# Performance work log

Measured on AMD Instinct MI355X. Metric: run time of the kernel, lower is better.

The kernel has to match this reference:

```python
import jax, jax.numpy as jnp
import numpy as np

HIDDEN = 4096
N_HEADS = 32
N_KV_HEADS = 8
HEAD_SIZE = HIDDEN // N_HEADS  # 128
ROPE_THETA = 10000.0
SEQ_LEN = 1024
BATCH = 4


def setup_inputs() -> dict:
    key = jax.random.key(0)
    k1, k2, k3 = jax.random.split(key, 3)
    scale = 1.0 / np.sqrt(HIDDEN)
    hidden_states = jax.random.normal(k1, (BATCH * SEQ_LEN, HIDDEN), dtype=jnp.float32)
    w_qkv = jax.random.normal(k2, ((N_HEADS + 2 * N_KV_HEADS) * HEAD_SIZE, HIDDEN), dtype=jnp.float32) * scale
    w_o = jax.random.normal(k3, (HIDDEN, N_HEADS * HEAD_SIZE), dtype=jnp.float32) * scale
    return {"hidden_states": hidden_states, "w_qkv": w_qkv, "w_o": w_o, "seq_len": SEQ_LEN}


def _rope(x, pos, theta):
    # x: [B, S, H, D]; pos: [S] absolute positions; rotate-half (LLAMA/NeoX) style
    d = x.shape[-1]
    inv_freq = 1.0 / (theta ** (jnp.arange(0, d, 2, dtype=jnp.float32) / d))  # [D/2]
    ang = pos.astype(jnp.float32)[:, None] * inv_freq[None, :]  # [S, D/2]
    cos = jnp.cos(ang)[None, :, None, :]
    sin = jnp.sin(ang)[None, :, None, :]
    x1, x2 = jnp.split(x, 2, axis=-1)
    return jnp.concatenate([x1 * cos - x2 * sin, x2 * cos + x1 * sin], axis=-1)


def reference(hidden_states, w_qkv, w_o, seq_len):
    total, hidden = hidden_states.shape
    B = total // seq_len
    hd = HEAD_SIZE
    # fused QKV projection (bias-free), split like the torch module
    qkv = hidden_states @ w_qkv.T  # [T, (H+2K)*hd]
    q, k, v = jnp.split(qkv, [N_HEADS * hd, (N_HEADS + N_KV_HEADS) * hd], axis=1)
    q = q.reshape(B, seq_len, N_HEADS, hd)
    k = k.reshape(B, seq_len, N_KV_HEADS, hd)
    v = v.reshape(B, seq_len, N_KV_HEADS, hd)
    # inline RoPE (ROPE_LLAMA) on q and k at absolute positions
    pos = jnp.arange(seq_len)
    q = _rope(q, pos, ROPE_THETA)
    k = _rope(k, pos, ROPE_THETA)
    # GQA: map each q head to its kv head (kv_head_mapping = repeat_interleave)
    groups = N_HEADS // N_KV_HEADS
    k = jnp.repeat(k, groups, axis=2)  # [B, S, H, hd]
    v = jnp.repeat(v, groups, axis=2)
    scale = hd ** -0.5
    scores = jnp.einsum('bqhd,bkhd->bhqk', q, k) * scale  # [B, H, S, S]
    causal = jnp.tril(jnp.ones((seq_len, seq_len), dtype=bool))
    scores = jnp.where(causal[None, None], scores, jnp.finfo(scores.dtype).min)
    probs = jax.nn.softmax(scores, axis=-1)
    attn = jnp.einsum('bhqk,bkhd->bqhd', probs, v).reshape(total, N_HEADS * hd)
    return attn @ w_o.T  # [T, hidden]
```

## Files before the change

kernel.cpp:

```cpp
#include <hip/hip_runtime.h>


typedef short bf16x8 __attribute__((ext_vector_type(8)));
typedef short bf16x4 __attribute__((ext_vector_type(4)));
typedef float floatx4 __attribute__((ext_vector_type(4)));
typedef unsigned short u16x8 __attribute__((ext_vector_type(8)));

__device__ __forceinline__ unsigned short f2bf(float f) {
  unsigned u = __float_as_uint(f);
  u += 0x7FFFu + ((u >> 16) & 1u);
  return (unsigned short)(u >> 16);
}
__device__ __forceinline__ float bf2f(unsigned short h) {
  return __uint_as_float(((unsigned)h) << 16);
}

__device__ __forceinline__ void async16(const void* g, void* l) {
  __builtin_amdgcn_global_load_lds(
      (const __attribute__((address_space(1))) unsigned int*)g,
      (__attribute__((address_space(3))) unsigned int*)l, 16, 0, 0);
}

__global__ void cvt_f32_bf16(const float4* __restrict__ in,
                             u16x8* __restrict__ out, int n8) {
  int i = blockIdx.x * 256 + threadIdx.x;
  if (i < n8) {
    float4 a = in[2 * i], b = in[2 * i + 1];
    u16x8 o;
    o[0] = f2bf(a.x); o[1] = f2bf(a.y); o[2] = f2bf(a.z); o[3] = f2bf(a.w);
    o[4] = f2bf(b.x); o[5] = f2bf(b.y); o[6] = f2bf(b.z); o[7] = f2bf(b.w);
    out[i] = o;
  }
}

template <int OUT_BF16>
__global__ __launch_bounds__(512, 2) void gemm256(
    const unsigned short* __restrict__ A, const unsigned short* __restrict__ B,
    void* __restrict__ Cout, int M, int N, int K, int n0) {
  __shared__ __align__(16) unsigned short As[4][8192];
  __shared__ __align__(16) unsigned short Bs[4][8192];
  const int tid = threadIdx.x;
  const int wave = tid >> 6, lane = tid & 63;
  const int wm = wave >> 2, wn = wave & 3;
  const int l16 = lane & 15, c4 = lane >> 4;
  const int bm = blockIdx.y << 8, bn = (blockIdx.x << 8) + n0;

  int afOff[8], bfOff[4];
#pragma unroll
  for (int mi = 0; mi < 8; ++mi) {
    int r = wm * 128 + mi * 16 + l16;
    int pr = r >> 1, l8 = ((r & 1) << 2) | c4;
    afOff[mi] = pr * 128 + ((l8 ^ (pr & 7)) << 4);
  }
#pragma unroll
  for (int ni = 0; ni < 4; ++ni) {
    int r = wn * 64 + ni * 16 + l16;
    int pr = r >> 1, l8 = ((r & 1) << 2) | c4;
    bfOff[ni] = pr * 128 + ((l8 ^ (pr & 7)) << 4);
  }

  const int sp = lane >> 3;
  const int l8s = (lane & 7) ^ sp;
  const int so = l8s >> 2, sc = (l8s & 3) << 3;
  const unsigned short* aS0 = A + (size_t)(bm + wave * 16 + sp * 2 + so) * K + sc;
  const unsigned short* aS1 = A + (size_t)(bm + (wave + 8) * 16 + sp * 2 + so) * K + sc;
  const unsigned short* bS0 = B + (size_t)(bn + wave * 16 + sp * 2 + so) * K + sc;
  const unsigned short* bS1 = B + (size_t)(bn + (wave + 8) * 16 + sp * 2 + so) * K + sc;
  const int dst0 = wave * 1024, dst1 = (wave + 8) * 1024;

  floatx4 acc[8][4];
#pragma unroll
  for (int mi = 0; mi < 8; ++mi)
#pragma unroll
    for (int ni = 0; ni < 4; ++ni) acc[mi][ni] = (floatx4){0.f, 0.f, 0.f, 0.f};

  const int NT = K >> 5;
  async16(aS0, (char*)As[0] + dst0);
  async16(aS1, (char*)As[0] + dst1);
  async16(bS0, (char*)Bs[0] + dst0);
  async16(bS1, (char*)Bs[0] + dst1);
  async16(aS0 + 32, (char*)As[1] + dst0);
  async16(aS1 + 32, (char*)As[1] + dst1);
  async16(bS0 + 32, (char*)Bs[1] + dst0);
  async16(bS1 + 32, (char*)Bs[1] + dst1);
  asm volatile("s_waitcnt vmcnt(4)" ::: "memory");
  __builtin_amdgcn_s_barrier();

  bf16x8 afq0[4], afq1[4], bfcA[4], bfcB[4];
#pragma unroll
  for (int i = 0; i < 4; ++i)
    afq0[i] = *(const bf16x8*)((const char*)As[0] + afOff[i]);
#pragma unroll
  for (int i = 0; i < 4; ++i)
    bfcA[i] = *(const bf16x8*)((const char*)Bs[0] + bfOff[i]);

  size_t koff = 64;

#define KTILE(T, BC, BN_)                                                     \
  {                                                                           \
    const char* aB = (const char*)As[(T) & 3];                                \
    const char* aN = (const char*)As[((T) + 1) & 3];                          \
    const char* bN = (const char*)Bs[((T) + 1) & 3];                          \
    char* aD = (char*)As[((T) + 2) & 3];                                      \
    char* bD = (char*)Bs[((T) + 2) & 3];                                      \
    _Pragma("unroll") for (int i = 0; i < 4; ++i)                             \
        afq1[i] = *(const bf16x8*)(aB + afOff[4 + i]);                        \
    async16(aS0 + koff, aD + dst0);                                           \
    async16(aS1 + koff, aD + dst1);                                           \
    __builtin_amdgcn_s_barrier();                                             \
    __builtin_amdgcn_s_setprio(1);                                            \
    _Pragma("unroll") for (int mi = 0; mi < 4; ++mi)                          \
        _Pragma("unroll") for (int ni = 0; ni < 4; ++ni)                      \
            acc[mi][ni] = __builtin_amdgcn_mfma_f32_16x16x32_bf16(            \
                afq0[mi], BC[ni], acc[mi][ni], 0, 0, 0);                      \
    __builtin_amdgcn_s_setprio(0);                                            \
    asm volatile("s_waitcnt vmcnt(2)" ::: "memory");   \
    __builtin_amdgcn_s_barrier();                     \
    _Pragma("unroll") for (int i = 0; i < 4; ++i)                             \
        afq0[i] = *(const bf16x8*)(aN + afOff[i]);                            \
    _Pragma("unroll") for (int i = 0; i < 4; ++i)                             \
        BN_[i] = *(const bf16x8*)(bN + bfOff[i]);                             \
    async16(bS0 + koff, bD + dst0);                                           \
    async16(bS1 + koff, bD + dst1);                                           \
    __builtin_amdgcn_s_barrier();                                             \
    __builtin_amdgcn_s_setprio(1);                                            \
    _Pragma("unroll") for (int mi = 0; mi < 4; ++mi)                          \
        _Pragma("unroll") for (int ni = 0; ni < 4; ++ni)                      \
            acc[4 + mi][ni] = __builtin_amdgcn_mfma_f32_16x16x32_bf16(        \
                afq1[mi], BC[ni], acc[4 + mi][ni], 0, 0, 0);                  \
    __builtin_amdgcn_s_setprio(0);                                            \
    __builtin_amdgcn_s_barrier();                                             \
    koff += 32;                                                               \
  }

  for (int t = 0; t < NT; t += 2) {
    KTILE(t, bfcA, bfcB);
    KTILE(t + 1, bfcB, bfcA);
  }
#undef KTILE

  const int col0 = bn + wn * 64 + l16;
#pragma unroll
  for (int mi = 0; mi < 8; ++mi) {
    const int row0 = bm + wm * 128 + mi * 16 + c4 * 4;
#pragma unroll
    for (int ni = 0; ni < 4; ++ni)
#pragma unroll
      for (int r = 0; r < 4; ++r) {
        if (OUT_BF16)
          ((unsigned short*)Cout)[(size_t)(row0 + r) * N + col0 + ni * 16] =
              f2bf(acc[mi][ni][r]);
        else
          ((float*)Cout)[(size_t)(row0 + r) * N + col0 + ni * 16] =
              acc[mi][ni][r];
      }
  }
}

__global__ void rope_k_kernel(unsigned short* __restrict__ qkv) {
  const int t = blockIdx.x;
  const int s = t & 1023;
  const int head = 32 + blockIdx.y * 4 + (threadIdx.x >> 6);
  const int d = threadIdx.x & 63;
  unsigned short* p = qkv + (size_t)t * 6144 + head * 128;
  float x1 = bf2f(p[d]), x2 = bf2f(p[d + 64]);
  float inv_freq = exp2f((float)d * -0.20762050593046015f);
  float ang = (float)s * inv_freq;
  float c, sn;
  __sincosf(ang, &sn, &c);
  p[d] = f2bf(x1 * c - x2 * sn);
  p[d + 64] = f2bf(x2 * c + x1 * sn);
}

__global__ __launch_bounds__(256, 3) void flash_attn(
    const unsigned short* __restrict__ qkv, unsigned short* __restrict__ aout) {
  const int pr = blockIdx.x;
  const int h = blockIdx.y, b = blockIdx.z;
  const int kh = h >> 2;
  const int tid = threadIdx.x;
  const int wave = tid >> 6, lane = tid & 63;
  const int quad = lane >> 4, l16 = lane & 15;

  __shared__ __align__(16) unsigned short Ks[64][136];
  __shared__ __align__(16) unsigned short Vt[128][68];
  __shared__ __align__(16) unsigned short Ps[64][68];

  const int krow = tid >> 4, kcol = (tid & 15) << 3;
  const int vrb = (tid & 15) << 2, vcol = (tid >> 4) << 3;
  const unsigned short* kp = qkv + (size_t)(b << 10) * 6144 + 4096 + kh * 128;
  const unsigned short* vp = qkv + (size_t)(b << 10) * 6144 + 5120 + kh * 128;

  for (int half = 0; half < 2; ++half) {
    const int qt = half ? pr : 15 - pr;
    const int q0 = qt << 6;

    bf16x8 qf[4];
    {
      const int qrow = q0 + wave * 16 + l16;
      const unsigned short* qp =
          qkv + (size_t)((b << 10) + qrow) * 6144 + h * 128 + quad * 8;
#pragma unroll
      for (int ks = 0; ks < 4; ++ks) qf[ks] = *(const bf16x8*)(qp + ks * 32);
      const float pos = (float)qrow;
      const float scale = 0.08838834764831845f;
#pragma unroll
      for (int ks = 0; ks < 2; ++ks)
#pragma unroll
        for (int e = 0; e < 8; ++e) {
          int d = ks * 32 + quad * 8 + e;
          float ang = pos * exp2f((float)d * -0.20762050593046015f);
          float c, sn;
          __sincosf(ang, &sn, &c);
          float x1 = bf2f((unsigned short)qf[ks][e]);
          float x2 = bf2f((unsigned short)qf[ks + 2][e]);
          qf[ks][e] = (short)f2bf((x1 * c - x2 * sn) * scale);
          qf[ks + 2][e] = (short)f2bf((x2 * c + x1 * sn) * scale);
        }
    }

    floatx4 o_acc[8];
#pragma unroll
    for (int i = 0; i < 8; ++i) o_acc[i] = (floatx4){0.f, 0.f, 0.f, 0.f};
    float l_lane[4] = {0.f, 0.f, 0.f, 0.f};

    bf16x8 kreg[4], vreg[4];
#pragma unroll
    for (int j = 0; j < 4; ++j)
      kreg[j] = *(const bf16x8*)(kp + (size_t)(krow + j * 16) * 6144 + kcol);
#pragma unroll
    for (int j = 0; j < 4; ++j)
      vreg[j] = *(const bf16x8*)(vp + (size_t)(vrb + j) * 6144 + vcol);

    for (int t = 0; t <= qt; ++t) {
      __syncthreads();
#pragma unroll
      for (int j = 0; j < 4; ++j)
        *(bf16x8*)&Ks[krow + j * 16][kcol] = kreg[j];
#pragma unroll
      for (int e = 0; e < 8; ++e) {
        bf16x4 w = {vreg[0][e], vreg[1][e], vreg[2][e], vreg[3][e]};
        *(bf16x4*)&Vt[vcol + e][vrb] = w;
      }
      __syncthreads();
      if (t < qt) {
        const size_t nb = (size_t)((t + 1) << 6) * 6144;
#pragma unroll
        for (int j = 0; j < 4; ++j)
          kreg[j] =
              *(const bf16x8*)(kp + nb + (size_t)(krow + j * 16) * 6144 + kcol);
#pragma unroll
        for (int j = 0; j < 4; ++j)
          vreg[j] = *(const bf16x8*)(vp + nb + (size_t)(vrb + j) * 6144 + vcol);
      }

      floatx4 sacc[4];
#pragma unroll
      for (int ni = 0; ni < 4; ++ni) sacc[ni] = (floatx4){0.f, 0.f, 0.f, 0.f};
#pragma unroll
      for (int ks = 0; ks < 4; ++ks)
#pragma unroll
        for (int ni = 0; ni < 4; ++ni) {
          bf16x8 kf = *(const bf16x8*)&Ks[ni * 16 + l16][ks * 32 + quad * 8];
          sacc[ni] = __builtin_amdgcn_mfma_f32_16x16x32_bf16(qf[ks], kf,
                                                             sacc[ni], 0, 0, 0);
        }

      const bool masked = (t == qt);
#pragma unroll
      for (int r = 0; r < 4; ++r) {
        float rs = 0.f;
#pragma unroll
        for (int ni = 0; ni < 4; ++ni) {
          float e = __expf(sacc[ni][r]);
          if (masked && (ni * 16 + l16) > (wave * 16 + quad * 4 + r)) e = 0.f;
          rs += e;
          Ps[wave * 16 + quad * 4 + r][ni * 16 + l16] = f2bf(e);
        }
        l_lane[r] += rs;
      }
      asm volatile("s_waitcnt lgkmcnt(0)" ::: "memory");

#pragma unroll
      for (int ks2 = 0; ks2 < 2; ++ks2) {
        bf16x8 pf = *(const bf16x8*)&Ps[wave * 16 + l16][ks2 * 32 + quad * 8];
#pragma unroll
        for (int n8 = 0; n8 < 8; ++n8) {
          bf16x8 vf = *(const bf16x8*)&Vt[n8 * 16 + l16][ks2 * 32 + quad * 8];
          o_acc[n8] = __builtin_amdgcn_mfma_f32_16x16x32_bf16(pf, vf, o_acc[n8],
                                                              0, 0, 0);
        }
      }
    }

#pragma unroll
    for (int r = 0; r < 4; ++r) {
      float l = l_lane[r];
#pragma unroll
      for (int off = 1; off < 16; off <<= 1) l += __shfl_xor(l, off, 64);
      float inv = 1.0f / l;
      int row = q0 + wave * 16 + quad * 4 + r;
      unsigned short* op = aout + (size_t)((b << 10) + row) * 4096 + h * 128;
#pragma unroll
      for (int n8 = 0; n8 < 8; ++n8)
        op[n8 * 16 + l16] = f2bf(o_acc[n8][r] * inv);
    }
  }
}

extern "C" void kernel_launch(void* const* d_in, const int* in_sizes, int n_in,
                              void* d_out, int out_size, void* d_ws,
                              size_t ws_size, hipStream_t stream) {
  const float* X = (const float*)d_in[0];
  const float* Wqkv = (const float*)d_in[1];
  const float* Wo = (const float*)d_in[2];
  (void)in_sizes; (void)n_in; (void)out_size; (void)ws_size;

  char* ws = (char*)d_ws;
  unsigned short* Wqkvb = (unsigned short*)ws;
  unsigned short* AttnB = (unsigned short*)ws;
  unsigned short* Xb = (unsigned short*)(ws + 50331648);
  unsigned short* Wob = (unsigned short*)(ws + 50331648);
  unsigned short* QKVb = (unsigned short*)(ws + 83886080);

  cvt_f32_bf16<<<8192, 256, 0, stream>>>((const float4*)X, (u16x8*)Xb, 2097152);
  cvt_f32_bf16<<<12288, 256, 0, stream>>>((const float4*)Wqkv, (u16x8*)Wqkvb, 3145728);
  gemm256<1><<<dim3(16, 16), 512, 0, stream>>>(Xb, Wqkvb, QKVb, 4096, 6144, 4096, 0);
  gemm256<1><<<dim3(8, 16), 512, 0, stream>>>(Xb, Wqkvb, QKVb, 4096, 6144, 4096, 4096);
  rope_k_kernel<<<dim3(4096, 2), 256, 0, stream>>>(QKVb);
  cvt_f32_bf16<<<8192, 256, 0, stream>>>((const float4*)Wo, (u16x8*)Wob, 2097152);
  flash_attn<<<dim3(8, 32, 4), 256, 0, stream>>>(QKVb, AttnB);
  gemm256<0><<<dim3(16, 16), 512, 0, stream>>>(AttnB, Wob, d_out, 4096, 4096, 4096, 0);
}
```

Baseline: 674.7 us.

## Rebalance flash-attention query tiles and merge QKV GEMM and convert launches

Flash attention now assigns 2-3 query tiles per block from a constant table so that 768 blocks carry roughly equal causal work, instead of 1024 blocks each pairing two tiles. The two split QKV GEMM launches become a single 24x16 grid, and the X and Wqkv fp32-to-bf16 conversions are fused into one kernel. The aim is to cut launch overhead and the partial-wave tail. The trade-off is fewer attention blocks, which may lower the latency hiding that comes from more resident work.

```diff
diff --git a/kernel.cpp b/kernel.cpp
--- a/kernel.cpp
+++ b/kernel.cpp
@@ -19,6 +19,24 @@
   __builtin_amdgcn_global_load_lds(
       (const __attribute__((address_space(1))) unsigned int*)g,
       (__attribute__((address_space(3))) unsigned int*)l, 16, 0, 0);
+}
+
+__global__ void cvt_xw(const float4* __restrict__ X,
+                       const float4* __restrict__ Wq,
+                       u16x8* __restrict__ Xb, u16x8* __restrict__ Wqb) {
+  const float4* src;
+  u16x8* dst;
+  int i;
+  if (blockIdx.x < 8192) {
+    src = X; dst = Xb; i = blockIdx.x * 256 + threadIdx.x;
+  } else {
+    src = Wq; dst = Wqb; i = (blockIdx.x - 8192) * 256 + threadIdx.x;
+  }
+  float4 a = src[2 * i], b = src[2 * i + 1];
+  u16x8 o;
+  o[0] = f2bf(a.x); o[1] = f2bf(a.y); o[2] = f2bf(a.z); o[3] = f2bf(a.w);
+  o[4] = f2bf(b.x); o[5] = f2bf(b.y); o[6] = f2bf(b.z); o[7] = f2bf(b.w);
+  dst[i] = o;
 }
 
 __global__ void cvt_f32_bf16(const float4* __restrict__ in,
@@ -36,14 +54,14 @@
 template <int OUT_BF16>
 __global__ __launch_bounds__(512, 2) void gemm256(
     const unsigned short* __restrict__ A, const unsigned short* __restrict__ B,
-    void* __restrict__ Cout, int M, int N, int K, int n0) {
+    void* __restrict__ Cout, int M, int N, int K) {
   __shared__ __align__(16) unsigned short As[4][8192];
   __shared__ __align__(16) unsigned short Bs[4][8192];
   const int tid = threadIdx.x;
   const int wave = tid >> 6, lane = tid & 63;
   const int wm = wave >> 2, wn = wave & 3;
   const int l16 = lane & 15, c4 = lane >> 4;
-  const int bm = blockIdx.y << 8, bn = (blockIdx.x << 8) + n0;
+  const int bm = blockIdx.y << 8, bn = blockIdx.x << 8;
 
   int afOff[8], bfOff[4];
 #pragma unroll
@@ -172,6 +190,9 @@
   p[d + 64] = f2bf(x2 * c + x1 * sn);
 }
 
+__device__ __constant__ int QTS[6][3] = {
+    {15, 4, 3}, {14, 5, 2}, {13, 6, 1}, {12, 7, 0}, {11, 8, -1}, {10, 9, -1}};
+
 __global__ __launch_bounds__(256, 3) void flash_attn(
     const unsigned short* __restrict__ qkv, unsigned short* __restrict__ aout) {
   const int pr = blockIdx.x;
@@ -190,8 +211,9 @@
   const unsigned short* kp = qkv + (size_t)(b << 10) * 6144 + 4096 + kh * 128;
   const unsigned short* vp = qkv + (size_t)(b << 10) * 6144 + 5120 + kh * 128;
 
-  for (int half = 0; half < 2; ++half) {
-    const int qt = half ? pr : 15 - pr;
+  for (int qi = 0; qi < 3; ++qi) {
+    const int qt = QTS[pr][qi];
+    if (qt < 0) break;
     const int q0 = qt << 6;
 
     bf16x8 qf[4];
@@ -322,12 +344,11 @@
   unsigned short* Wob = (unsigned short*)(ws + 50331648);
   unsigned short* QKVb = (unsigned short*)(ws + 83886080);
 
-  cvt_f32_bf16<<<8192, 256, 0, stream>>>((const float4*)X, (u16x8*)Xb, 2097152);
-  cvt_f32_bf16<<<12288, 256, 0, stream>>>((const float4*)Wqkv, (u16x8*)Wqkvb, 3145728);
-  gemm256<1><<<dim3(16, 16), 512, 0, stream>>>(Xb, Wqkvb, QKVb, 4096, 6144, 4096, 0);
-  gemm256<1><<<dim3(8, 16), 512, 0, stream>>>(Xb, Wqkvb, QKVb, 4096, 6144, 4096, 4096);
+  cvt_xw<<<20480, 256, 0, stream>>>((const float4*)X, (const float4*)Wqkv,
+                                    (u16x8*)Xb, (u16x8*)Wqkvb);
+  gemm256<1><<<dim3(24, 16), 512, 0, stream>>>(Xb, Wqkvb, QKVb, 4096, 6144, 4096);
   rope_k_kernel<<<dim3(4096, 2), 256, 0, stream>>>(QKVb);
   cvt_f32_bf16<<<8192, 256, 0, stream>>>((const float4*)Wo, (u16x8*)Wob, 2097152);
-  flash_attn<<<dim3(8, 32, 4), 256, 0, stream>>>(QKVb, AttnB);
-  gemm256<0><<<dim3(16, 16), 512, 0, stream>>>(AttnB, Wob, d_out, 4096, 4096, 4096, 0);
-}
+  flash_attn<<<dim3(6, 32, 4), 256, 0, stream>>>(QKVb, AttnB);
+  gemm256<0><<<dim3(16, 16), 512, 0, stream>>>(AttnB, Wob, d_out, 4096, 4096, 4096);
+}
```

After: 658.4 us. 2.4% less time.
